# Performance work log

Measured on AMD Instinct MI355X. Metric: run time of the kernel, lower is better.

## Reference

```python
import jax, jax.numpy as jnp
import numpy as np

# Lattice / model constants (from init_kwargs)
LX, LY = 12, 12
N = LX * LY
NH = 64              # GRU hidden units
K = 2                # local Hilbert-space dim (occupied / empty)
NSAMPLES = 4096
EPS = 1e-10


def setup_inputs() -> dict:
    key = jax.random.key(0)
    k1, k2, k3 = jax.random.split(key, 3)
    s_in = 1.0 / np.sqrt(K + NH)   # glorot-ish scale for input kernel
    s_rec = 1.0 / np.sqrt(NH)
    W = (jax.random.normal(k1, (K, 3 * NH)) * s_in).astype(jnp.float32)    # GRU input kernel
    U = (jax.random.normal(k2, (NH, 3 * NH)) * s_rec).astype(jnp.float32)  # GRU recurrent kernel
    b = jnp.zeros((2, 3 * NH), dtype=jnp.float32)   # reset_after: [input_bias, recurrent_bias]
    Wd = (jax.random.normal(k3, (NH, K)) * s_rec).astype(jnp.float32)      # Dense kernel
    bd = jnp.zeros((K,), dtype=jnp.float32)
    return {"nsamples": NSAMPLES, "W": W, "U": U, "b": b, "Wd": Wd, "bd": bd}


def _gru_cell(x, h, W, U, b):
    # TF2 Keras GRU cell, reset_after=True, tanh / sigmoid activations.
    xm = x @ W + b[0]                      # [ns, 3nh]
    hm = h @ U + b[1]                      # [ns, 3nh]
    xz, xr, xn = jnp.split(xm, 3, axis=1)
    hz, hr, hn = jnp.split(hm, 3, axis=1)
    z = jax.nn.sigmoid(xz + hz)            # update gate
    r = jax.nn.sigmoid(xr + hr)            # reset gate
    hh = jnp.tanh(xn + r * hn)             # candidate
    return z * h + (1.0 - z) * hh


def reference(nsamples, W, U, b, Wd, bd):
    keys = jax.random.split(jax.random.key(42), N)
    h0 = jnp.zeros((nsamples, NH), dtype=W.dtype)
    x0 = jnp.zeros((nsamples, K), dtype=W.dtype)   # 0.0 * one_hot(0)
    logP0 = jnp.zeros((nsamples,), dtype=W.dtype)

    def step(carry, k):
        h, x, logP = carry
        h = _gru_cell(x, h, W, U, b)
        probs = jax.nn.softmax(h @ Wd + bd, axis=-1)     # Dense with softmax activation
        logp = jnp.log(EPS + probs)                      # [ns, K]
        s = jax.random.categorical(k, logp, axis=-1)     # [ns] int sample
        x_new = jax.nn.one_hot(s, K, dtype=W.dtype)
        logP = logP + jnp.sum(logp * x_new, axis=1)
        return (h, x_new, logP), s

    (_, _, logP), samples = jax.lax.scan(step, (h0, x0, logP0), keys)
    samples = samples.T                                  # [ns, N]
    return samples, logP
```

## Files before the change

### kernel.cpp

```cpp
#include <hip/hip_runtime.h>
#include <cstdint>
#include <math.h>


#define NSAMP 4096
#define NSTEP 144
#define HID 64
#define CPB 2

typedef float v4f  __attribute__((ext_vector_type(4)));
typedef float v2f  __attribute__((ext_vector_type(2)));

__device__ __forceinline__ void threefry2x32(uint32_t k0, uint32_t k1,
                                             uint32_t x0, uint32_t x1,
                                             uint32_t& o0, uint32_t& o1) {
  const uint32_t ks0 = k0, ks1 = k1, ks2 = k0 ^ k1 ^ 0x1BD11BDAu;
  x0 += ks0; x1 += ks1;
#define TF_ROUND(d) { x0 += x1; x1 = (x1 << (d)) | (x1 >> (32 - (d))); x1 ^= x0; }
  TF_ROUND(13) TF_ROUND(15) TF_ROUND(26) TF_ROUND(6)
  x0 += ks1; x1 += ks2 + 1u;
  TF_ROUND(17) TF_ROUND(29) TF_ROUND(16) TF_ROUND(24)
  x0 += ks2; x1 += ks0 + 2u;
  TF_ROUND(13) TF_ROUND(15) TF_ROUND(26) TF_ROUND(6)
  x0 += ks0; x1 += ks1 + 3u;
  TF_ROUND(17) TF_ROUND(29) TF_ROUND(16) TF_ROUND(24)
  x0 += ks1; x1 += ks2 + 4u;
  TF_ROUND(13) TF_ROUND(15) TF_ROUND(26) TF_ROUND(6)
  x0 += ks2; x1 += ks0 + 5u;
#undef TF_ROUND
  o0 = x0; o1 = x1;
}

__device__ __forceinline__ float fsig(float x) {
  return __builtin_amdgcn_rcpf(1.0f + __expf(-x));
}
__device__ __forceinline__ float ftanh(float x) {
  const float e = __expf(2.0f * x);
  return 1.0f - 2.0f * __builtin_amdgcn_rcpf(e + 1.0f);
}

#define PKFMA_LO(acc, h2, up) \
  asm("v_pk_fma_f32 %0, %1, %2, %0 op_sel_hi:[1,0,1]" \
      : "+v"(acc) : "v"(h2), "v"(up));
#define PKFMA_HI(acc, h2, up) \
  asm("v_pk_fma_f32 %0, %1, %2, %0 op_sel:[0,1,0] op_sel_hi:[1,1,1]" \
      : "+v"(acc) : "v"(h2), "v"(up));

template <int CTRL>
__device__ __forceinline__ float dpp_add(float v) {
  union { float f; int i; } c; c.f = v;
  union { int i; float f; } r;
  r.i = __builtin_amdgcn_mov_dpp(c.i, CTRL, 0xF, 0xF, true);
  return v + r.f;
}
#define DPP_XOR1 0xB1
#define DPP_XOR2 0x4E
#define DPP_XOR4 0x141
#define DPP_XOR8 0x140

__global__ __launch_bounds__(64, 1) void vmc_kernel(
    const float* __restrict__ W, const float* __restrict__ U,
    const float* __restrict__ B, const float* __restrict__ Wd,
    const float* __restrict__ Bd, float* __restrict__ out) {
  const int j = threadIdx.x;
  const int s_base = blockIdx.x * CPB;

  __shared__ __align__(16) float2 hsh2[HID];
  __shared__ __align__(16) float2 upairs[32 * HID];
  __shared__ uint2 kkeys[NSTEP];
  __shared__ float gsh[CPB * 2 * NSTEP];

#pragma unroll 1
  for (int t = j; t < NSTEP; t += HID) {
    uint32_t o0, o1;
    threefry2x32(0u, 42u, 0u, (uint32_t)t, o0, o1);
    kkeys[t].x = o0; kkeys[t].y = o1;
  }
  hsh2[j] = float2{0.0f, 0.0f};
  __syncthreads();

#pragma unroll 1
  for (int id = j; id < CPB * 2 * NSTEP; id += HID) {
    const int c = id / 288;
    const int idx = id - c * 288;
    const uint2 kt = kkeys[idx >> 1];
    const uint32_t i = 2u * (uint32_t)(s_base + c) + (uint32_t)(idx & 1);
    uint32_t o0, o1;
    threefry2x32(kt.x, kt.y, 0u, i, o0, o1);
    const uint32_t bits = o0 ^ o1;
    union { uint32_t u; float f; } cv; cv.u = (bits >> 9) | 0x3F800000u;
    float uf = cv.f - 1.0f;
    uf = fmaxf(uf, 1.17549435e-38f);
    const float inner = (float)log((double)uf);
    gsh[id] = -(float)log((double)(-inner));
  }
  __syncthreads();

  v2f uq[96];
#define STAGE_GATE(g) \
  { _Pragma("unroll") \
    for (int p = 0; p < 32; ++p) { \
      float2 w; \
      w.x = U[(2*p + 0) * 192 + (g)*64 + j]; \
      w.y = U[(2*p + 1) * 192 + (g)*64 + j]; \
      upairs[p * HID + j] = w; \
    } \
    __syncthreads(); \
    _Pragma("unroll") \
    for (int p = 0; p < 32; ++p) \
      uq[(g)*32 + p] = *(const v2f*)&upairs[p * HID + j]; \
    __syncthreads(); }
  STAGE_GATE(0)
  STAGE_GATE(1)
  STAGE_GATE(2)
#undef STAGE_GATE
  asm volatile("" ::: "memory");

  const float b1z = B[192 + j], b1r = B[256 + j], b1n = B[320 + j];
  const float b0z = B[j],       b0r = B[64 + j],  b0n = B[128 + j];
  const float xW0z = W[j]       + b0z, xW1z = W[192 + j] + b0z;
  const float xW0r = W[64 + j]  + b0r, xW1r = W[256 + j] + b0r;
  const float xW0n = W[128 + j] + b0n, xW1n = W[320 + j] + b0n;
  const float wdd = Wd[2*j + 1] - Wd[2*j];
  const float bdd = Bd[1] - Bd[0];

  float ha = 0.0f, hb_ = 0.0f;
  float logPa = 0.0f, logPb = 0.0f;
  float axz = b0z, axr = b0r, axn = b0n;
  float bxz = b0z, bxr = b0r, bxn = b0n;
  v2f hz2 = {0.f, 0.f}, hr2 = {0.f, 0.f}, hn2 = {0.f, 0.f};

  for (int t = 0; t < NSTEP; ++t) {
    {
      const float az = axz + (hz2.x + b1z), ar = axr + (hr2.x + b1r);
      const float zz = fsig(az), rr = fsig(ar);
      const float hh = ftanh(axn + rr * (hn2.x + b1n));
      ha = zz * ha + (1.0f - zz) * hh;
    }
    {
      const float az = bxz + (hz2.y + b1z), ar = bxr + (hr2.y + b1r);
      const float zz = fsig(az), rr = fsig(ar);
      const float hh = ftanh(bxn + rr * (hn2.y + b1n));
      hb_ = zz * hb_ + (1.0f - zz) * hh;
    }
    hsh2[j] = float2{ha, hb_};

    float da = ha * wdd, db = hb_ * wdd;
    da = dpp_add<DPP_XOR1>(da); db = dpp_add<DPP_XOR1>(db);
    da = dpp_add<DPP_XOR2>(da); db = dpp_add<DPP_XOR2>(db);
    da = dpp_add<DPP_XOR4>(da); db = dpp_add<DPP_XOR4>(db);
    da = dpp_add<DPP_XOR8>(da); db = dpp_add<DPP_XOR8>(db);
    da += __shfl_xor(da, 16, 64); db += __shfl_xor(db, 16, 64);
    da += __shfl_xor(da, 32, 64); db += __shfl_xor(db, 32, 64);

    int sma, smb;
    {
      const float d = da + bdd;
      const float p1 = fsig(d), p0 = fsig(-d);
      const float lp0 = __logf(1e-10f + p0);
      const float lp1 = __logf(1e-10f + p1);
      const float g0 = gsh[2*t], g1 = gsh[2*t + 1];
      sma = (lp1 + g1) > (lp0 + g0);
      logPa += sma ? lp1 : lp0;
      axz = sma ? xW1z : xW0z;
      axr = sma ? xW1r : xW0r;
      axn = sma ? xW1n : xW0n;
    }
    {
      const float d = db + bdd;
      const float p1 = fsig(d), p0 = fsig(-d);
      const float lp0 = __logf(1e-10f + p0);
      const float lp1 = __logf(1e-10f + p1);
      const float g0 = gsh[288 + 2*t], g1 = gsh[288 + 2*t + 1];
      smb = (lp1 + g1) > (lp0 + g0);
      logPb += smb ? lp1 : lp0;
      bxz = smb ? xW1z : xW0z;
      bxr = smb ? xW1r : xW0r;
      bxn = smb ? xW1n : xW0n;
    }
    if (j == 0) {
      out[(s_base + 0) * NSTEP + t] = sma ? 1.0f : 0.0f;
      out[(s_base + 1) * NSTEP + t] = smb ? 1.0f : 0.0f;
    }

    hz2 = v2f{0.f, 0.f}; hr2 = v2f{0.f, 0.f}; hn2 = v2f{0.f, 0.f};
#define DOTC(c_) \
    { const v4f hA = *(const v4f*)&hsh2[(c_)*4]; \
      const v4f hB = *(const v4f*)&hsh2[(c_)*4 + 2]; \
      const v2f h0  = __builtin_shufflevector(hA, hA, 0, 1); \
      const v2f h1  = __builtin_shufflevector(hA, hA, 2, 3); \
      const v2f h2_ = __builtin_shufflevector(hB, hB, 0, 1); \
      const v2f h3  = __builtin_shufflevector(hB, hB, 2, 3); \
      PKFMA_LO(hz2, h0,  uq[0*32 + 2*(c_)])     PKFMA_LO(hr2, h0,  uq[1*32 + 2*(c_)])     PKFMA_LO(hn2, h0,  uq[2*32 + 2*(c_)]) \
      PKFMA_HI(hz2, h1,  uq[0*32 + 2*(c_)])     PKFMA_HI(hr2, h1,  uq[1*32 + 2*(c_)])     PKFMA_HI(hn2, h1,  uq[2*32 + 2*(c_)]) \
      PKFMA_LO(hz2, h2_, uq[0*32 + 2*(c_) + 1]) PKFMA_LO(hr2, h2_, uq[1*32 + 2*(c_) + 1]) PKFMA_LO(hn2, h2_, uq[2*32 + 2*(c_) + 1]) \
      PKFMA_HI(hz2, h3,  uq[0*32 + 2*(c_) + 1]) PKFMA_HI(hr2, h3,  uq[1*32 + 2*(c_) + 1]) PKFMA_HI(hn2, h3,  uq[2*32 + 2*(c_) + 1]) }
    DOTC(0)  DOTC(1)  DOTC(2)  DOTC(3)
    DOTC(4)  DOTC(5)  DOTC(6)  DOTC(7)
    DOTC(8)  DOTC(9)  DOTC(10) DOTC(11)
    DOTC(12) DOTC(13) DOTC(14) DOTC(15)
#undef DOTC
  }

  if (j == 0) {
    *(float2*)&out[NSAMP * NSTEP + s_base] = float2{logPa, logPb};
  }
}

extern "C" void kernel_launch(void* const* d_in, const int* in_sizes, int n_in,
                              void* d_out, int out_size, void* d_ws, size_t ws_size,
                              hipStream_t stream) {
  const float* W  = (const float*)d_in[1];
  const float* U  = (const float*)d_in[2];
  const float* B  = (const float*)d_in[3];
  const float* Wd = (const float*)d_in[4];
  const float* Bd = (const float*)d_in[5];
  vmc_kernel<<<dim3(NSAMP / CPB), dim3(HID), 0, stream>>>(W, U, B, Wd, Bd, (float*)d_out);
}
```

Baseline: 303.7 us.

## Process four chains per wavefront with four waves per block

Each wavefront now carries four sample chains instead of two, and each block packs four wavefronts, so the grid shrinks from 2048 to 256 blocks of 256 threads. U is staged once per block into LDS as float4 quads and held in 48 v4f registers. Gumbel noise is generated in two halves to bound LDS use. The goal is to amortise the per-step U register reuse over more chains and raise instruction-level parallelism in the latency-bound recurrence. The cost is more registers per thread, fewer blocks (256 on 256 CUs, so roughly one wave per SIMD), and a mid-loop block barrier at step 72.

```diff
diff --git a/kernel.cpp b/kernel.cpp
--- a/kernel.cpp
+++ b/kernel.cpp
@@ -6,10 +6,13 @@
 #define NSAMP 4096
 #define NSTEP 144
 #define HID 64
-#define CPB 2
-
-typedef float v4f  __attribute__((ext_vector_type(4)));
-typedef float v2f  __attribute__((ext_vector_type(2)));
+#define CPW 4
+#define WPB 4
+#define CPBLK (CPW * WPB)
+#define HSTEP 72
+
+typedef float v4f __attribute__((ext_vector_type(4)));
+typedef float v2f __attribute__((ext_vector_type(2)));
 
 __device__ __forceinline__ void threefry2x32(uint32_t k0, uint32_t k1,
                                              uint32_t x0, uint32_t x1,
@@ -58,152 +61,177 @@
 #define DPP_XOR4 0x141
 #define DPP_XOR8 0x140
 
-__global__ __launch_bounds__(64, 1) void vmc_kernel(
+__global__ __launch_bounds__(256, 1) void vmc_kernel(
     const float* __restrict__ W, const float* __restrict__ U,
     const float* __restrict__ B, const float* __restrict__ Wd,
     const float* __restrict__ Bd, float* __restrict__ out) {
-  const int j = threadIdx.x;
-  const int s_base = blockIdx.x * CPB;
-
-  __shared__ __align__(16) float2 hsh2[HID];
-  __shared__ __align__(16) float2 upairs[32 * HID];
-  __shared__ uint2 kkeys[NSTEP];
-  __shared__ float gsh[CPB * 2 * NSTEP];
-
-#pragma unroll 1
-  for (int t = j; t < NSTEP; t += HID) {
+  const int tid = threadIdx.x;
+  const int j = tid & 63;
+  const int w = tid >> 6;
+  const int s_blk = blockIdx.x * CPBLK;
+  const int s0 = s_blk + w * CPW;
+
+  __shared__ __align__(16) float4 uq4[3 * 16 * 64];
+  __shared__ __align__(16) float4 hsh4[WPB * HID];
+  __shared__ __align__(16) uint2 kkeys[NSTEP];
+  __shared__ __align__(16) float gsh[CPBLK * 2 * HSTEP];
+
+  for (int t = tid; t < NSTEP; t += 256) {
     uint32_t o0, o1;
     threefry2x32(0u, 42u, 0u, (uint32_t)t, o0, o1);
     kkeys[t].x = o0; kkeys[t].y = o1;
   }
-  hsh2[j] = float2{0.0f, 0.0f};
   __syncthreads();
 
+  for (int vv = tid; vv < 3 * 16 * 64; vv += 256) {
+    const int v = (vv & ~63) | ((vv ^ 1) & 63);
+    const int g = v >> 10, rem = v & 1023, q = rem >> 6;
+    const int col = (g << 6) | (rem & 63);
+    float4 x;
+    x.x = U[(4 * q + 0) * 192 + col];
+    x.y = U[(4 * q + 1) * 192 + col];
+    x.z = U[(4 * q + 2) * 192 + col];
+    x.w = U[(4 * q + 3) * 192 + col];
+    uq4[v] = x;
+  }
+
+#define STAGE_GSH(TB) \
+  for (int id = tid; id < CPBLK * 2 * HSTEP; id += 256) { \
+    const int c16 = id / 144, r = id - c16 * 144; \
+    const uint2 kt = kkeys[(TB) + (r >> 1)]; \
+    const uint32_t i = 2u * (uint32_t)(s_blk + c16) + (uint32_t)(r & 1); \
+    uint32_t o0, o1; \
+    threefry2x32(kt.x, kt.y, 0u, i, o0, o1); \
+    const uint32_t bits = o0 ^ o1; \
+    union { uint32_t u; float f; } cv; cv.u = (bits >> 9) | 0x3F800000u; \
+    float uf = cv.f - 1.0f; \
+    uf = fmaxf(uf, 1.17549435e-38f); \
+    const float inner = (float)log((double)uf); \
+    gsh[id] = -(float)log((double)(-inner)); \
+  }
+  STAGE_GSH(0)
+  __syncthreads();
+
+  v4f uqr[48];
+#pragma unroll
+  for (int g = 0; g < 3; ++g)
+#pragma unroll
+    for (int q = 0; q < 16; ++q)
+      uqr[g * 16 + q] = *(const v4f*)&uq4[g * 1024 + q * 64 + j];
+
+  const float b1z = B[192 + j], b1r = B[256 + j], b1n = B[320 + j];
+  const float b0z = B[j], b0r = B[64 + j], b0n = B[128 + j];
+  const float xW0z = W[j] + b0z,        xW1z = W[192 + j] + b0z;
+  const float xW0r = W[64 + j] + b0r,   xW1r = W[256 + j] + b0r;
+  const float xW0n = W[128 + j] + b0n,  xW1n = W[320 + j] + b0n;
+  const float wdd = Wd[2 * j + 1] - Wd[2 * j];
+  const float bdd = Bd[1] - Bd[0];
+
+  const float4* hw = &hsh4[w * HID];
+  float4* hww = &hsh4[w * HID];
+  const float* gw = &gsh[(w * CPW) * (2 * HSTEP)];
+
+  float axz[4], axr[4], axn[4], logP[4], hcur[4];
+#pragma unroll
+  for (int cc = 0; cc < 4; ++cc) {
+    axz[cc] = b0z; axr[cc] = b0r; axn[cc] = b0n;
+    logP[cc] = 0.0f; hcur[cc] = 0.0f;
+  }
+  v2f hzAB = {0.f, 0.f}, hzCD = {0.f, 0.f};
+  v2f hrAB = {0.f, 0.f}, hrCD = {0.f, 0.f};
+  v2f hnAB = {0.f, 0.f}, hnCD = {0.f, 0.f};
+
 #pragma unroll 1
-  for (int id = j; id < CPB * 2 * NSTEP; id += HID) {
-    const int c = id / 288;
-    const int idx = id - c * 288;
-    const uint2 kt = kkeys[idx >> 1];
-    const uint32_t i = 2u * (uint32_t)(s_base + c) + (uint32_t)(idx & 1);
-    uint32_t o0, o1;
-    threefry2x32(kt.x, kt.y, 0u, i, o0, o1);
-    const uint32_t bits = o0 ^ o1;
-    union { uint32_t u; float f; } cv; cv.u = (bits >> 9) | 0x3F800000u;
-    float uf = cv.f - 1.0f;
-    uf = fmaxf(uf, 1.17549435e-38f);
-    const float inner = (float)log((double)uf);
-    gsh[id] = -(float)log((double)(-inner));
-  }
-  __syncthreads();
-
-  v2f uq[96];
-#define STAGE_GATE(g) \
-  { _Pragma("unroll") \
-    for (int p = 0; p < 32; ++p) { \
-      float2 w; \
-      w.x = U[(2*p + 0) * 192 + (g)*64 + j]; \
-      w.y = U[(2*p + 1) * 192 + (g)*64 + j]; \
-      upairs[p * HID + j] = w; \
-    } \
-    __syncthreads(); \
-    _Pragma("unroll") \
-    for (int p = 0; p < 32; ++p) \
-      uq[(g)*32 + p] = *(const v2f*)&upairs[p * HID + j]; \
-    __syncthreads(); }
-  STAGE_GATE(0)
-  STAGE_GATE(1)
-  STAGE_GATE(2)
-#undef STAGE_GATE
-  asm volatile("" ::: "memory");
-
-  const float b1z = B[192 + j], b1r = B[256 + j], b1n = B[320 + j];
-  const float b0z = B[j],       b0r = B[64 + j],  b0n = B[128 + j];
-  const float xW0z = W[j]       + b0z, xW1z = W[192 + j] + b0z;
-  const float xW0r = W[64 + j]  + b0r, xW1r = W[256 + j] + b0r;
-  const float xW0n = W[128 + j] + b0n, xW1n = W[320 + j] + b0n;
-  const float wdd = Wd[2*j + 1] - Wd[2*j];
-  const float bdd = Bd[1] - Bd[0];
-
-  float ha = 0.0f, hb_ = 0.0f;
-  float logPa = 0.0f, logPb = 0.0f;
-  float axz = b0z, axr = b0r, axn = b0n;
-  float bxz = b0z, bxr = b0r, bxn = b0n;
-  v2f hz2 = {0.f, 0.f}, hr2 = {0.f, 0.f}, hn2 = {0.f, 0.f};
-
   for (int t = 0; t < NSTEP; ++t) {
-    {
-      const float az = axz + (hz2.x + b1z), ar = axr + (hr2.x + b1r);
-      const float zz = fsig(az), rr = fsig(ar);
-      const float hh = ftanh(axn + rr * (hn2.x + b1n));
-      ha = zz * ha + (1.0f - zz) * hh;
+    asm volatile("" ::: "memory");
+    if (t == HSTEP) {
+      __syncthreads();
+      STAGE_GSH(HSTEP)
+      __syncthreads();
     }
-    {
-      const float az = bxz + (hz2.y + b1z), ar = bxr + (hr2.y + b1r);
-      const float zz = fsig(az), rr = fsig(ar);
-      const float hh = ftanh(bxn + rr * (hn2.y + b1n));
-      hb_ = zz * hb_ + (1.0f - zz) * hh;
+
+#define GATE(cc, hz_, hr_, hn_) { \
+      const float az = axz[cc] + ((hz_) + b1z), ar = axr[cc] + ((hr_) + b1r); \
+      const float zz = fsig(az), rr = fsig(ar); \
+      const float hh = ftanh(axn[cc] + rr * ((hn_) + b1n)); \
+      hcur[cc] = zz * hcur[cc] + (1.0f - zz) * hh; }
+    GATE(0, hzAB.x, hrAB.x, hnAB.x)
+    GATE(1, hzAB.y, hrAB.y, hnAB.y)
+    GATE(2, hzCD.x, hrCD.x, hnCD.x)
+    GATE(3, hzCD.y, hrCD.y, hnCD.y)
+#undef GATE
+    hww[j] = make_float4(hcur[0], hcur[1], hcur[2], hcur[3]);
+
+    const int dt = (t < HSTEP) ? t : (t - HSTEP);
+    const float* gt = gw + 2 * dt;
+    int smv[4];
+#define CHAIN_DEC(cc) { \
+      float d_ = hcur[cc] * wdd; \
+      d_ = dpp_add<DPP_XOR1>(d_); d_ = dpp_add<DPP_XOR2>(d_); \
+      d_ = dpp_add<DPP_XOR4>(d_); d_ = dpp_add<DPP_XOR8>(d_); \
+      d_ += __shfl_xor(d_, 16, 64); d_ += __shfl_xor(d_, 32, 64); \
+      const float d = d_ + bdd; \
+      const float p1 = fsig(d), p0 = fsig(-d); \
+      const float lp0 = __logf(1e-10f + p0); \
+      const float lp1 = __logf(1e-10f + p1); \
+      const float g0 = gt[(cc) * 144], g1 = gt[(cc) * 144 + 1]; \
+      const int sm = (lp1 + g1) > (lp0 + g0); \
+      logP[cc] += sm ? lp1 : lp0; \
+      axz[cc] = sm ? xW1z : xW0z; \
+      axr[cc] = sm ? xW1r : xW0r; \
+      axn[cc] = sm ? xW1n : xW0n; \
+      smv[cc] = sm; }
+    CHAIN_DEC(0) CHAIN_DEC(1) CHAIN_DEC(2) CHAIN_DEC(3)
+#undef CHAIN_DEC
+    if (j == 0) {
+      out[(s0 + 0) * NSTEP + t] = smv[0] ? 1.0f : 0.0f;
+      out[(s0 + 1) * NSTEP + t] = smv[1] ? 1.0f : 0.0f;
+      out[(s0 + 2) * NSTEP + t] = smv[2] ? 1.0f : 0.0f;
+      out[(s0 + 3) * NSTEP + t] = smv[3] ? 1.0f : 0.0f;
     }
-    hsh2[j] = float2{ha, hb_};
-
-    float da = ha * wdd, db = hb_ * wdd;
-    da = dpp_add<DPP_XOR1>(da); db = dpp_add<DPP_XOR1>(db);
-    da = dpp_add<DPP_XOR2>(da); db = dpp_add<DPP_XOR2>(db);
-    da = dpp_add<DPP_XOR4>(da); db = dpp_add<DPP_XOR4>(db);
-    da = dpp_add<DPP_XOR8>(da); db = dpp_add<DPP_XOR8>(db);
-    da += __shfl_xor(da, 16, 64); db += __shfl_xor(db, 16, 64);
-    da += __shfl_xor(da, 32, 64); db += __shfl_xor(db, 32, 64);
-
-    int sma, smb;
-    {
-      const float d = da + bdd;
-      const float p1 = fsig(d), p0 = fsig(-d);
-      const float lp0 = __logf(1e-10f + p0);
-      const float lp1 = __logf(1e-10f + p1);
-      const float g0 = gsh[2*t], g1 = gsh[2*t + 1];
-      sma = (lp1 + g1) > (lp0 + g0);
-      logPa += sma ? lp1 : lp0;
-      axz = sma ? xW1z : xW0z;
-      axr = sma ? xW1r : xW0r;
-      axn = sma ? xW1n : xW0n;
-    }
-    {
-      const float d = db + bdd;
-      const float p1 = fsig(d), p0 = fsig(-d);
-      const float lp0 = __logf(1e-10f + p0);
-      const float lp1 = __logf(1e-10f + p1);
-      const float g0 = gsh[288 + 2*t], g1 = gsh[288 + 2*t + 1];
-      smb = (lp1 + g1) > (lp0 + g0);
-      logPb += smb ? lp1 : lp0;
-      bxz = smb ? xW1z : xW0z;
-      bxr = smb ? xW1r : xW0r;
-      bxn = smb ? xW1n : xW0n;
-    }
-    if (j == 0) {
-      out[(s_base + 0) * NSTEP + t] = sma ? 1.0f : 0.0f;
-      out[(s_base + 1) * NSTEP + t] = smb ? 1.0f : 0.0f;
-    }
-
-    hz2 = v2f{0.f, 0.f}; hr2 = v2f{0.f, 0.f}; hn2 = v2f{0.f, 0.f};
-#define DOTC(c_) \
-    { const v4f hA = *(const v4f*)&hsh2[(c_)*4]; \
-      const v4f hB = *(const v4f*)&hsh2[(c_)*4 + 2]; \
-      const v2f h0  = __builtin_shufflevector(hA, hA, 0, 1); \
-      const v2f h1  = __builtin_shufflevector(hA, hA, 2, 3); \
-      const v2f h2_ = __builtin_shufflevector(hB, hB, 0, 1); \
-      const v2f h3  = __builtin_shufflevector(hB, hB, 2, 3); \
-      PKFMA_LO(hz2, h0,  uq[0*32 + 2*(c_)])     PKFMA_LO(hr2, h0,  uq[1*32 + 2*(c_)])     PKFMA_LO(hn2, h0,  uq[2*32 + 2*(c_)]) \
-      PKFMA_HI(hz2, h1,  uq[0*32 + 2*(c_)])     PKFMA_HI(hr2, h1,  uq[1*32 + 2*(c_)])     PKFMA_HI(hn2, h1,  uq[2*32 + 2*(c_)]) \
-      PKFMA_LO(hz2, h2_, uq[0*32 + 2*(c_) + 1]) PKFMA_LO(hr2, h2_, uq[1*32 + 2*(c_) + 1]) PKFMA_LO(hn2, h2_, uq[2*32 + 2*(c_) + 1]) \
-      PKFMA_HI(hz2, h3,  uq[0*32 + 2*(c_) + 1]) PKFMA_HI(hr2, h3,  uq[1*32 + 2*(c_) + 1]) PKFMA_HI(hn2, h3,  uq[2*32 + 2*(c_) + 1]) }
+
+    hzAB = v2f{0.f, 0.f}; hzCD = v2f{0.f, 0.f};
+    hrAB = v2f{0.f, 0.f}; hrCD = v2f{0.f, 0.f};
+    hnAB = v2f{0.f, 0.f}; hnCD = v2f{0.f, 0.f};
+#define SV2(x, a, b) __builtin_shufflevector(x, x, a, b)
+#define DOTC(c_) { \
+      const v4f uz4 = uqr[(c_)]; \
+      const v4f ur4 = uqr[16 + (c_)]; \
+      const v4f un4 = uqr[32 + (c_)]; \
+      const v4f h40 = *(const v4f*)&hw[(c_) * 4 + 0]; \
+      const v4f h41 = *(const v4f*)&hw[(c_) * 4 + 1]; \
+      const v4f h42 = *(const v4f*)&hw[(c_) * 4 + 2]; \
+      const v4f h43 = *(const v4f*)&hw[(c_) * 4 + 3]; \
+      const v2f uz01 = SV2(uz4, 0, 1), uz23 = SV2(uz4, 2, 3); \
+      const v2f ur01 = SV2(ur4, 0, 1), ur23 = SV2(ur4, 2, 3); \
+      const v2f un01 = SV2(un4, 0, 1), un23 = SV2(un4, 2, 3); \
+      { const v2f hab = SV2(h40, 0, 1), hcd = SV2(h40, 2, 3); \
+        PKFMA_LO(hzAB, hab, uz01) PKFMA_LO(hzCD, hcd, uz01) \
+        PKFMA_LO(hrAB, hab, ur01) PKFMA_LO(hrCD, hcd, ur01) \
+        PKFMA_LO(hnAB, hab, un01) PKFMA_LO(hnCD, hcd, un01) } \
+      { const v2f hab = SV2(h41, 0, 1), hcd = SV2(h41, 2, 3); \
+        PKFMA_HI(hzAB, hab, uz01) PKFMA_HI(hzCD, hcd, uz01) \
+        PKFMA_HI(hrAB, hab, ur01) PKFMA_HI(hrCD, hcd, ur01) \
+        PKFMA_HI(hnAB, hab, un01) PKFMA_HI(hnCD, hcd, un01) } \
+      { const v2f hab = SV2(h42, 0, 1), hcd = SV2(h42, 2, 3); \
+        PKFMA_LO(hzAB, hab, uz23) PKFMA_LO(hzCD, hcd, uz23) \
+        PKFMA_LO(hrAB, hab, ur23) PKFMA_LO(hrCD, hcd, ur23) \
+        PKFMA_LO(hnAB, hab, un23) PKFMA_LO(hnCD, hcd, un23) } \
+      { const v2f hab = SV2(h43, 0, 1), hcd = SV2(h43, 2, 3); \
+        PKFMA_HI(hzAB, hab, uz23) PKFMA_HI(hzCD, hcd, uz23) \
+        PKFMA_HI(hrAB, hab, ur23) PKFMA_HI(hrCD, hcd, ur23) \
+        PKFMA_HI(hnAB, hab, un23) PKFMA_HI(hnCD, hcd, un23) } }
     DOTC(0)  DOTC(1)  DOTC(2)  DOTC(3)
     DOTC(4)  DOTC(5)  DOTC(6)  DOTC(7)
     DOTC(8)  DOTC(9)  DOTC(10) DOTC(11)
     DOTC(12) DOTC(13) DOTC(14) DOTC(15)
 #undef DOTC
+#undef SV2
   }
 
   if (j == 0) {
-    *(float2*)&out[NSAMP * NSTEP + s_base] = float2{logPa, logPb};
+    *(float4*)&out[NSAMP * NSTEP + s0] =
+        make_float4(logP[0], logP[1], logP[2], logP[3]);
   }
 }
 
@@ -215,5 +243,6 @@
   const float* B  = (const float*)d_in[3];
   const float* Wd = (const float*)d_in[4];
   const float* Bd = (const float*)d_in[5];
-  vmc_kernel<<<dim3(NSAMP / CPB), dim3(HID), 0, stream>>>(W, U, B, Wd, Bd, (float*)d_out);
-}
+  vmc_kernel<<<dim3(NSAMP / CPBLK), dim3(WPB * HID), 0, stream>>>(
+      W, U, B, Wd, Bd, (float*)d_out);
+}
```

Result: slower. 358.2 us (+17.9%).
